# Kernel tuning notes

Measured on AMD Instinct MI355X. Metric: run time of the kernel, lower is better.

## Reference

```python
import jax, jax.numpy as jnp
import numpy as np

NUM_BINS = 512  # 8 levels per RGB channel: (R>>5)<<6 + (G>>5)<<3 + (B>>5)


def _color_histograms(frames):
    # frames: [B, T, H, W, 3] int32, values in [0, 256)
    B, T, H, W, _ = frames.shape
    f = frames.reshape(B * T, H * W, 3)
    R, G, Bc = f[:, :, 0], f[:, :, 1], f[:, :, 2]
    binned = ((R >> 5) << 6) + ((G >> 5) << 3) + (Bc >> 5)  # [BT, HW] in [0,512)
    prefix = (jnp.arange(B * T, dtype=jnp.int32) << 9)[:, None]  # frame offset (512 bins/frame)
    idx = (binned + prefix).reshape(-1)
    hist = jnp.zeros(B * T * NUM_BINS, dtype=jnp.int32).at[idx].add(jnp.int32(1))
    hist = hist.reshape(B, T, NUM_BINS).astype(jnp.float32)
    # F.normalize(p=2, dim=2, eps=1e-12)
    norm = jnp.sqrt(jnp.sum(hist * hist, axis=2, keepdims=True))
    return hist / jnp.maximum(norm, 1e-12)


def setup_inputs() -> dict:
    key = jax.random.key(0)
    k1, k2, k3 = jax.random.split(key, 3)
    frames = jax.random.randint(k1, (16, 256, 64, 64, 3), 0, 256, dtype=jnp.int32)
    fc_w = jax.random.normal(k2, (128, 101), dtype=jnp.float32) * 0.1
    fc_b = jax.random.normal(k3, (128,), dtype=jnp.float32) * 0.01
    return {"frames": frames, "fc_w": fc_w, "fc_b": fc_b}


def reference(frames, fc_w, fc_b):
    lookup_window = fc_w.shape[1]
    half = (lookup_window - 1) // 2
    x = _color_histograms(frames)  # [B, T, 512]
    B, T, _ = x.shape
    sim = jnp.einsum('btd,bsd->bts', x, x)  # [B, T, T]
    sim_padded = jnp.pad(sim, ((0, 0), (0, 0), (half, half)))  # [B, T, T+W-1]
    t_idx = jnp.arange(T)[:, None]                    # [T, 1]
    l_idx = t_idx + jnp.arange(lookup_window)[None, :]  # [T, W]
    windowed = sim_padded[:, t_idx, l_idx]            # [B, T, W]
    return jax.nn.relu(jnp.einsum('btw,ow->bto', windowed, fc_w) + fc_b)
```

## Files before the change

kernel.cpp:

```cpp
#include <hip/hip_runtime.h>
#include <hip/hip_bf16.h>

#define NUM_BINS 512
#define T_LEN 256
#define B_LEN 16
#define WIN 101
#define HALF 50
#define NOUT 128

typedef __attribute__((ext_vector_type(8))) short short8;
typedef __attribute__((ext_vector_type(4))) float f32x4;

__device__ __forceinline__ unsigned short f2bf(float f) {
    unsigned u = __float_as_uint(f);
    u += 0x7fff + ((u >> 16) & 1);
    return (unsigned short)(u >> 16);
}

__global__ __launch_bounds__(256) void hist_kernel(const int* __restrict__ frames,
                                                   __hip_bfloat16* __restrict__ xout) {
    __shared__ int hist[NUM_BINS];
    __shared__ float red[4];
    const int f = blockIdx.x;
    const int tid = threadIdx.x;

    hist[tid] = 0;
    hist[tid + 256] = 0;
    __syncthreads();

    const int* base = frames + (size_t)f * 12288;
    #pragma unroll 4
    for (int i = 0; i < 16; ++i) {
        const int p = i * 256 + tid;
        int3 v = *(const int3*)(base + (size_t)p * 3);
        atomicAdd(&hist[((v.x >> 5) << 6) | ((v.y >> 5) << 3) | (v.z >> 5)], 1);
    }
    __syncthreads();

    const int h0 = hist[tid];
    const int h1 = hist[tid + 256];
    float ss = (float)h0 * (float)h0 + (float)h1 * (float)h1;
    #pragma unroll
    for (int off = 32; off; off >>= 1) ss += __shfl_down(ss, off, 64);
    const int lane = tid & 63;
    const int wave = tid >> 6;
    if (lane == 0) red[wave] = ss;
    __syncthreads();
    const float tot = red[0] + red[1] + red[2] + red[3];
    const float inv = 1.0f / sqrtf(tot);
    __hip_bfloat16* xrow = xout + (size_t)f * NUM_BINS;
    xrow[tid] = __float2bfloat16((float)h0 * inv);
    xrow[tid + 256] = __float2bfloat16((float)h1 * inv);
}

__global__ __launch_bounds__(512) void simfc_kernel(const unsigned short* __restrict__ x,
                                                    const float* __restrict__ fc_w,
                                                    const float* __restrict__ fc_b,
                                                    float* __restrict__ out) {
    __shared__ float sim_lds[16 * 132];
    __shared__ unsigned short win_lds[16 * 136];

    const int bid = blockIdx.x;
    const int b = bid & 15;
    const int tt = bid >> 4;
    const int t0 = tt * 16;
    const int tid = threadIdx.x;
    const int lane = tid & 63;
    const int wave = tid >> 6;
    const int l15 = lane & 15;
    const int kg = lane >> 4;

    const unsigned short* xb = x + (size_t)b * T_LEN * NUM_BINS;

    {
        f32x4 acc = {0.f, 0.f, 0.f, 0.f};
        const short8 zero8 = {0, 0, 0, 0, 0, 0, 0, 0};
        const int rowA = t0 + l15;
        const int rb = t0 - HALF + 16 * wave + l15;
        const bool vv = (rb >= 0) && (rb < T_LEN);
        const int rc = min(max(rb, 0), T_LEN - 1);
        const unsigned short* pa = xb + (size_t)rowA * NUM_BINS + kg * 8;
        const unsigned short* ps = xb + (size_t)rc * NUM_BINS + kg * 8;
        #pragma unroll
        for (int ks = 0; ks < 16; ++ks) {
            short8 a  = *(const short8*)(pa + ks * 32);
            short8 bb = *(const short8*)(ps + ks * 32);
            bb = vv ? bb : zero8;
            acc = __builtin_amdgcn_mfma_f32_16x16x32_bf16(a, bb, acc, 0, 0, 0);
        }
        #pragma unroll
        for (int r = 0; r < 4; ++r)
            sim_lds[(kg * 4 + r) * 132 + wave * 16 + l15] = acc[r];
    }
    __syncthreads();

    if (tid < 256) {
        const int i = tid >> 4;
        const int w8 = (tid & 15) * 8;
        short8 v;
        #pragma unroll
        for (int e = 0; e < 8; ++e) {
            const int w = w8 + e;
            const float fv = (w < WIN) ? sim_lds[i * 132 + i + w] : 0.0f;
            v[e] = (short)f2bf(fv);
        }
        *(short8*)(&win_lds[i * 136 + w8]) = v;
    }
    __syncthreads();

    {
        f32x4 o0 = {0.f, 0.f, 0.f, 0.f};
        const int o = wave * 16 + l15;
        const float* pw = fc_w + o * WIN;
        #pragma unroll
        for (int ks = 0; ks < 4; ++ks) {
            const int wbase = ks * 32 + kg * 8;
            short8 a = *(const short8*)(&win_lds[l15 * 136 + wbase]);
            short8 b0;
            #pragma unroll
            for (int e = 0; e < 8; ++e) {
                const int w = wbase + e;
                b0[e] = (short)((w < WIN) ? f2bf(pw[w]) : (unsigned short)0);
            }
            o0 = __builtin_amdgcn_mfma_f32_16x16x32_bf16(a, b0, o0, 0, 0, 0);
        }
        const float bias = fc_b[o];
        float* ob = out + ((size_t)b * T_LEN + t0) * NOUT;
        #pragma unroll
        for (int r = 0; r < 4; ++r)
            ob[(kg * 4 + r) * NOUT + o] = fmaxf(o0[r] + bias, 0.0f);
    }
}

extern "C" void kernel_launch(void* const* d_in, const int* in_sizes, int n_in,
                              void* d_out, int out_size, void* d_ws, size_t ws_size,
                              hipStream_t stream) {
    const int* frames = (const int*)d_in[0];
    const float* fc_w = (const float*)d_in[1];
    const float* fc_b = (const float*)d_in[2];
    float* out = (float*)d_out;
    __hip_bfloat16* x = (__hip_bfloat16*)d_ws;

    hist_kernel<<<B_LEN * T_LEN, 256, 0, stream>>>(frames, x);
    simfc_kernel<<<B_LEN * T_LEN / 16, 512, 0, stream>>>((const unsigned short*)x, fc_w, fc_b, out);
}
```

Measured before the change: 44.86 us.

## Process two frames per histogram block and pre-swizzle fc weights to bf16

The histogram kernel now handles two frames per block with separate LDS histograms, which halves the block count and amortizes setup and synchronisation. Eight extra blocks convert fc_w to bf16 in the MFMA operand layout and store it in workspace, so the sim/FC kernel loads one short8 per step instead of eight scattered floats with per-element conversion. The trade-offs are less block-level parallelism in the bandwidth-bound histogram pass and a dependency on a workspace offset at 4 MB.

```diff
diff --git a/kernel.cpp b/kernel.cpp
--- a/kernel.cpp
+++ b/kernel.cpp
@@ -17,44 +17,89 @@
     return (unsigned short)(u >> 16);
 }
 
-__global__ __launch_bounds__(256) void hist_kernel(const int* __restrict__ frames,
-                                                   __hip_bfloat16* __restrict__ xout) {
-    __shared__ int hist[NUM_BINS];
-    __shared__ float red[4];
-    const int f = blockIdx.x;
+__device__ __forceinline__ int bin3(int3 v) {
+    return ((v.x >> 5) << 6) | ((v.y >> 5) << 3) | (v.z >> 5);
+}
+
+__global__ __launch_bounds__(256, 8) void hist_kernel(const int* __restrict__ frames,
+                                                      const float* __restrict__ fc_w,
+                                                      __hip_bfloat16* __restrict__ xout,
+                                                      unsigned short* __restrict__ fcswz) {
     const int tid = threadIdx.x;
+    const int bid = blockIdx.x;
 
-    hist[tid] = 0;
-    hist[tid + 256] = 0;
+    if (bid >= 2048) {
+        const int base = (bid - 2048) * 2048 + tid * 8;
+        const int l15 = (base >> 3) & 15;
+        const int kg = (base >> 7) & 3;
+        const int ks = (base >> 9) & 3;
+        const int og = base >> 11;
+        const int o = og * 16 + l15;
+        short8 v;
+        #pragma unroll
+        for (int e = 0; e < 8; ++e) {
+            const int w = ks * 32 + kg * 8 + e;
+            v[e] = (short)((w < WIN) ? f2bf(fc_w[o * WIN + w]) : (unsigned short)0);
+        }
+        *(short8*)(fcswz + base) = v;
+        return;
+    }
+
+    __shared__ int hist[2][NUM_BINS];
+    __shared__ float red[2][4];
+
+    hist[0][tid] = 0; hist[0][tid + 256] = 0;
+    hist[1][tid] = 0; hist[1][tid + 256] = 0;
     __syncthreads();
 
-    const int* base = frames + (size_t)f * 12288;
-    #pragma unroll 4
+    const int* base0 = frames + (size_t)bid * 24576;
+    #pragma unroll 8
     for (int i = 0; i < 16; ++i) {
-        const int p = i * 256 + tid;
-        int3 v = *(const int3*)(base + (size_t)p * 3);
-        atomicAdd(&hist[((v.x >> 5) << 6) | ((v.y >> 5) << 3) | (v.z >> 5)], 1);
+        int3 v = *(const int3*)(base0 + (i * 256 + tid) * 3);
+        atomicAdd(&hist[0][bin3(v)], 1);
     }
     __syncthreads();
 
-    const int h0 = hist[tid];
-    const int h1 = hist[tid + 256];
-    float ss = (float)h0 * (float)h0 + (float)h1 * (float)h1;
-    #pragma unroll
-    for (int off = 32; off; off >>= 1) ss += __shfl_down(ss, off, 64);
+    const int* base1 = base0 + 12288;
+    #pragma unroll 8
+    for (int i = 0; i < 16; ++i) {
+        int3 v = *(const int3*)(base1 + (i * 256 + tid) * 3);
+        atomicAdd(&hist[1][bin3(v)], 1);
+    }
+
     const int lane = tid & 63;
     const int wave = tid >> 6;
-    if (lane == 0) red[wave] = ss;
+
+    const int a0 = hist[0][tid];
+    const int a1 = hist[0][tid + 256];
+    float ss0 = (float)a0 * (float)a0 + (float)a1 * (float)a1;
+    #pragma unroll
+    for (int off = 32; off; off >>= 1) ss0 += __shfl_down(ss0, off, 64);
+    if (lane == 0) red[0][wave] = ss0;
     __syncthreads();
-    const float tot = red[0] + red[1] + red[2] + red[3];
-    const float inv = 1.0f / sqrtf(tot);
-    __hip_bfloat16* xrow = xout + (size_t)f * NUM_BINS;
-    xrow[tid] = __float2bfloat16((float)h0 * inv);
-    xrow[tid + 256] = __float2bfloat16((float)h1 * inv);
+    {
+        const float inv = 1.0f / sqrtf(red[0][0] + red[0][1] + red[0][2] + red[0][3]);
+        __hip_bfloat16* xrow = xout + (size_t)(bid * 2) * NUM_BINS;
+        xrow[tid] = __float2bfloat16((float)a0 * inv);
+        xrow[tid + 256] = __float2bfloat16((float)a1 * inv);
+    }
+    const int b0 = hist[1][tid];
+    const int b1 = hist[1][tid + 256];
+    float ss1 = (float)b0 * (float)b0 + (float)b1 * (float)b1;
+    #pragma unroll
+    for (int off = 32; off; off >>= 1) ss1 += __shfl_down(ss1, off, 64);
+    if (lane == 0) red[1][wave] = ss1;
+    __syncthreads();
+    {
+        const float inv = 1.0f / sqrtf(red[1][0] + red[1][1] + red[1][2] + red[1][3]);
+        __hip_bfloat16* xrow = xout + (size_t)(bid * 2 + 1) * NUM_BINS;
+        xrow[tid] = __float2bfloat16((float)b0 * inv);
+        xrow[tid + 256] = __float2bfloat16((float)b1 * inv);
+    }
 }
 
 __global__ __launch_bounds__(512) void simfc_kernel(const unsigned short* __restrict__ x,
-                                                    const float* __restrict__ fc_w,
+                                                    const unsigned short* __restrict__ fcswz,
                                                     const float* __restrict__ fc_b,
                                                     float* __restrict__ out) {
     __shared__ float sim_lds[16 * 132];
@@ -111,17 +156,10 @@
     {
         f32x4 o0 = {0.f, 0.f, 0.f, 0.f};
         const int o = wave * 16 + l15;
-        const float* pw = fc_w + o * WIN;
         #pragma unroll
         for (int ks = 0; ks < 4; ++ks) {
-            const int wbase = ks * 32 + kg * 8;
-            short8 a = *(const short8*)(&win_lds[l15 * 136 + wbase]);
-            short8 b0;
-            #pragma unroll
-            for (int e = 0; e < 8; ++e) {
-                const int w = wbase + e;
-                b0[e] = (short)((w < WIN) ? f2bf(pw[w]) : (unsigned short)0);
-            }
+            short8 a = *(const short8*)(&win_lds[l15 * 136 + ks * 32 + kg * 8]);
+            short8 b0 = *(const short8*)(fcswz + ((((wave * 4 + ks) * 4 + kg) * 16 + l15) * 8));
             o0 = __builtin_amdgcn_mfma_f32_16x16x32_bf16(a, b0, o0, 0, 0, 0);
         }
         const float bias = fc_b[o];
@@ -140,7 +178,8 @@
     const float* fc_b = (const float*)d_in[2];
     float* out = (float*)d_out;
     __hip_bfloat16* x = (__hip_bfloat16*)d_ws;
+    unsigned short* fcswz = (unsigned short*)((char*)d_ws + (4 << 20));
 
-    hist_kernel<<<B_LEN * T_LEN, 256, 0, stream>>>(frames, x);
-    simfc_kernel<<<B_LEN * T_LEN / 16, 512, 0, stream>>>((const unsigned short*)x, fc_w, fc_b, out);
+    hist_kernel<<<2048 + 8, 256, 0, stream>>>(frames, fc_w, x, fcswz);
+    simfc_kernel<<<256, 512, 0, stream>>>((const unsigned short*)x, fcswz, fc_b, out);
 }
```

New measurement: 44.44 us. Within noise of the previous version (-0.9%).
